# Optimization experiments

Hardware: AMD Instinct MI355X
Metric: run time of the kernel (lower is better)

Reference implementation:

```python
import jax, jax.numpy as jnp
import numpy as np

HEIGHT = 10
IN_DIM = 256
OUT_DIM = 16
BATCH = 65536


def _and_weight(height):
    # Fixed +/-1 tree-structured routing matrix [leaf_nodes, int_nodes]
    int_nodes = 2 ** height - 1
    leaf = 2 ** height
    w = np.zeros((leaf, int_nodes), dtype=np.float32)
    for i in range(height):
        num = 2 ** i
        start = num - 1
        for j in range(start, start + num):
            rb = leaf // num * (j - start)
            rm = rb + leaf // (2 * num)
            re = rb + leaf // num
            w[rb:rm, j] = 1.0
            w[rm:re, j] = -1.0
    return jnp.asarray(w)


def setup_inputs() -> dict:
    key = jax.random.key(0)
    k0, k1, k2, k3 = jax.random.split(key, 4)
    int_nodes = 2 ** HEIGHT - 1
    leaf = 2 ** HEIGHT
    return {
        "x": jax.random.normal(k0, (BATCH, IN_DIM), jnp.float32),
        "W_pred": jax.random.normal(k1, (int_nodes, IN_DIM), jnp.float32) / np.float32(np.sqrt(IN_DIM)),
        "b_pred": jnp.zeros((int_nodes,), jnp.float32),
        "W_or": jax.random.normal(k2, (OUT_DIM, leaf), jnp.float32) / np.float32(np.sqrt(leaf)),
        "action_stds": jax.random.normal(k3, (OUT_DIM, leaf), jnp.float32),
    }


def reference(x, W_pred, b_pred, W_or, action_stds):
    # predicate linear: [B, int_nodes]
    pred_z = x @ W_pred.T + b_pred
    # ScaleBinarizer1 (STE): scale = mean |z| per sample, binarize to {0, fac}
    fac = jax.lax.stop_gradient(jnp.mean(jnp.abs(pred_z), axis=-1, keepdims=True))
    hard = jnp.where(pred_z >= 0, fac, jnp.zeros_like(fac))
    pred_bin = pred_z + jax.lax.stop_gradient(hard - pred_z)  # straight-through
    pred_a = 2.0 * pred_bin - fac  # +/- fac (sign of pred_z scaled)
    # fixed tree AND layer: [B, leaf]
    W_and = _and_weight(HEIGHT)
    and_z = pred_a @ W_and.T
    and_a = jax.nn.softmax(and_z, axis=-1)
    # Sparser1 (STE): hard one-hot of the argmax leaf
    onehot = jax.nn.one_hot(jnp.argmax(and_a, axis=-1), and_a.shape[-1], dtype=and_a.dtype)
    and_a = and_a + jax.lax.stop_gradient(onehot - and_a)
    # OR layer + softmax over classes
    or_z = and_a @ W_or.T  # [B, out_dim]
    out = jax.nn.softmax(or_z, axis=-1)
    # per-action std: sum over leaves of and_a * action_stds, clamped
    std = jnp.clip(jnp.einsum("bl,ol->bo", and_a, action_stds), -20.0, 2.0)
    return out, std
```

## Files before the change

kernel.cpp:

```cpp
#include <hip/hip_runtime.h>
#include <stdint.h>


#define BATCH   65536
#define IN_DIM  256
#define NLEVEL  10
#define NLEAF   1024
#define OUT_DIM 16
#define EPS_TIE 0.02f
#define WB_U32  (1023 * 128)

#define DPP_QUAD_XOR1   0xB1
#define DPP_QUAD_XOR2   0x4E
#define DPP_HALF_MIRROR 0x141

template <int CTRL>
__device__ __forceinline__ float dpp_xfer(float v) {
    return __int_as_float(__builtin_amdgcn_update_dpp(
        0, __float_as_int(v), CTRL, 0xf, 0xf, true));
}
__device__ __forceinline__ float group8_sum(float v) {
    v += dpp_xfer<DPP_QUAD_XOR1>(v);
    v += dpp_xfer<DPP_QUAD_XOR2>(v);
    v += dpp_xfer<DPP_HALF_MIRROR>(v);
    return v;
}
__device__ __forceinline__ float group8_max(float v) {
    v = fmaxf(v, dpp_xfer<DPP_QUAD_XOR1>(v));
    v = fmaxf(v, dpp_xfer<DPP_QUAD_XOR2>(v));
    v = fmaxf(v, dpp_xfer<DPP_HALF_MIRROR>(v));
    return v;
}

__device__ __forceinline__ float blo(uint32_t u) { return __uint_as_float(u << 16); }
__device__ __forceinline__ float bhi(uint32_t u) { return __uint_as_float(u & 0xffff0000u); }

__device__ __forceinline__ uint32_t pkbf(float a, float b) {
    uint32_t ua = __float_as_uint(a), ub = __float_as_uint(b);
    uint32_t ra = (ua + 0x7fffu + ((ua >> 16) & 1u)) >> 16;
    uint32_t rb = (ub + 0x7fffu + ((ub >> 16) & 1u)) >> 16;
    return ra | (rb << 16);
}

__global__ __launch_bounds__(256) void dgt_prep(
    const float* __restrict__ W, uint32_t* __restrict__ Wb)
{
    int i = blockIdx.x * 256 + threadIdx.x;
    if (i < WB_U32) Wb[i] = pkbf(W[2 * i], W[2 * i + 1]);
}

__device__ __forceinline__ int tree_sign_f64(
    const float* __restrict__ xrow, const float* __restrict__ wrow,
    float bias, int l)
{
    double A0 = 0.0, A1 = 0.0, A2 = 0.0, A3 = 0.0;
    #pragma unroll
    for (int k = 0; k < 4; ++k) {
        float4 xa = *reinterpret_cast<const float4*>(xrow + k * 64 + l * 8);
        float4 xb = *reinterpret_cast<const float4*>(xrow + k * 64 + l * 8 + 4);
        float4 wa = *reinterpret_cast<const float4*>(wrow + k * 64 + l * 8);
        float4 wb = *reinterpret_cast<const float4*>(wrow + k * 64 + l * 8 + 4);
        A0 += (double)xa.x * (double)wa.x; A1 += (double)xa.y * (double)wa.y;
        A2 += (double)xa.z * (double)wa.z; A3 += (double)xa.w * (double)wa.w;
        A0 += (double)xb.x * (double)wb.x; A1 += (double)xb.y * (double)wb.y;
        A2 += (double)xb.z * (double)wb.z; A3 += (double)xb.w * (double)wb.w;
    }
    double Z = (A0 + A1) + (A2 + A3);
    #pragma unroll
    for (int off = 4; off > 0; off >>= 1)
        Z += __shfl_xor(Z, off, 64);
    Z += (double)bias;
    return (Z < 0.0) ? 1 : 0;
}

__global__ __launch_bounds__(256, 3) void dgt_b16(
    const float* __restrict__ x,
    const uint32_t* __restrict__ Wb,
    const float* __restrict__ W_pred,
    const float* __restrict__ b_pred,
    const float* __restrict__ W_or,
    const float* __restrict__ a_std,
    float* __restrict__ out)
{
    const int lane = threadIdx.x & 63;
    const int wid  = threadIdx.x >> 6;
    const int l    = lane & 7;
    const int g    = lane >> 3;
    const int sample = blockIdx.x * 32 + wid * 8 + g;

    const float* xrow = x + (size_t)sample * IN_DIM;
    uint32_t p0, p1, p2, p3, p4, p5, p6, p7, p8, p9, p10, p11, p12, p13, p14, p15;
    {
        float4 a0 = *reinterpret_cast<const float4*>(xrow +   0 + l * 8);
        float4 b0 = *reinterpret_cast<const float4*>(xrow +   4 + l * 8);
        float4 a1 = *reinterpret_cast<const float4*>(xrow +  64 + l * 8);
        float4 b1 = *reinterpret_cast<const float4*>(xrow +  68 + l * 8);
        p0 = pkbf(a0.x, a0.y); p1 = pkbf(a0.z, a0.w);
        p2 = pkbf(b0.x, b0.y); p3 = pkbf(b0.z, b0.w);
        p4 = pkbf(a1.x, a1.y); p5 = pkbf(a1.z, a1.w);
        p6 = pkbf(b1.x, b1.y); p7 = pkbf(b1.z, b1.w);
        float4 a2 = *reinterpret_cast<const float4*>(xrow + 128 + l * 8);
        float4 b2 = *reinterpret_cast<const float4*>(xrow + 132 + l * 8);
        float4 a3 = *reinterpret_cast<const float4*>(xrow + 192 + l * 8);
        float4 b3 = *reinterpret_cast<const float4*>(xrow + 196 + l * 8);
        p8  = pkbf(a2.x, a2.y); p9  = pkbf(a2.z, a2.w);
        p10 = pkbf(b2.x, b2.y); p11 = pkbf(b2.z, b2.w);
        p12 = pkbf(a3.x, a3.y); p13 = pkbf(a3.z, a3.w);
        p14 = pkbf(b3.x, b3.y); p15 = pkbf(b3.z, b3.w);
    }

    int node = 0, pos = 0;

    #pragma unroll
    for (int lvl = 0; lvl < NLEVEL; ++lvl) {
        const uint32_t* wb = Wb + (size_t)node * 128;
        float bcur = b_pred[node];

        uint4 A0 = *reinterpret_cast<const uint4*>(wb +  0 + l * 4);
        uint4 A1 = *reinterpret_cast<const uint4*>(wb + 32 + l * 4);
        uint4 B0 = *reinterpret_cast<const uint4*>(wb + 64 + l * 4);
        uint4 B1 = *reinterpret_cast<const uint4*>(wb + 96 + l * 4);

        float a0 = 0.f, a1 = 0.f, a2 = 0.f, a3 = 0.f;
#define FMAU(U, P)                                          \
        a0 += blo(U) * blo(P); a1 += bhi(U) * bhi(P);
#define FMA4(UQ, Pa, Pb, Pc, Pd)                            \
        FMAU(UQ.x, Pa) FMAU(UQ.y, Pb) FMAU(UQ.z, Pc) FMAU(UQ.w, Pd)
        FMA4(A0, p0,  p1,  p2,  p3)
        FMA4(A1, p4,  p5,  p6,  p7)
        FMA4(B0, p8,  p9,  p10, p11)
        FMA4(B1, p12, p13, p14, p15)
#undef FMA4
#undef FMAU

        float z = group8_sum((a0 + a1) + (a2 + a3)) + bcur;

        int right;
        if (__builtin_expect(fabsf(z) >= EPS_TIE, 1))
            right = (z < 0.f) ? 1 : 0;
        else
            right = tree_sign_f64(xrow, W_pred + (size_t)node * IN_DIM,
                                  bcur, l);

        pos  = 2 * pos + right;
        node = 2 * node + 1 + right;
    }
    const int leaf = pos;

    float zx = W_or[(size_t)(2 * l)     * NLEAF + leaf];
    float zy = W_or[(size_t)(2 * l + 1) * NLEAF + leaf];
    float m  = group8_max(fmaxf(zx, zy));
    float ex = __expf(zx - m), ey = __expf(zy - m);
    float s  = group8_sum(ex + ey);
    *reinterpret_cast<float2*>(out + (size_t)sample * OUT_DIM + 2 * l) =
        make_float2(ex / s, ey / s);

    float dx = a_std[(size_t)(2 * l)     * NLEAF + leaf];
    float dy = a_std[(size_t)(2 * l + 1) * NLEAF + leaf];
    *reinterpret_cast<float2*>(out + (size_t)BATCH * OUT_DIM
                               + (size_t)sample * OUT_DIM + 2 * l) =
        make_float2(fminf(fmaxf(dx, -20.f), 2.f),
                    fminf(fmaxf(dy, -20.f), 2.f));
}

__device__ __forceinline__ int tree_sign_f64_r8(
    float4 x0, float4 x1, float4 x2, float4 x3,
    float4 x4, float4 x5, float4 x6, float4 x7,
    const float* wrow, float bias, int l)
{
    double A0 = 0.0, A1 = 0.0, A2 = 0.0, A3 = 0.0;
#define ACC64(K, XV)                                                        \
    {                                                                       \
        float4 w = *reinterpret_cast<const float4*>(wrow + (K)*32 + l * 4); \
        A0 += (double)XV.x * (double)w.x; A1 += (double)XV.y * (double)w.y; \
        A2 += (double)XV.z * (double)w.z; A3 += (double)XV.w * (double)w.w; \
    }
    ACC64(0, x0) ACC64(1, x1) ACC64(2, x2) ACC64(3, x3)
    ACC64(4, x4) ACC64(5, x5) ACC64(6, x6) ACC64(7, x7)
#undef ACC64
    double Z = (A0 + A1) + (A2 + A3);
    #pragma unroll
    for (int off = 4; off > 0; off >>= 1)
        Z += __shfl_xor(Z, off, 64);
    Z += (double)bias;
    return (Z < 0.0) ? 1 : 0;
}

__global__ __launch_bounds__(256, 2) void dgt_f32(
    const float* __restrict__ x,
    const float* __restrict__ W_pred,
    const float* __restrict__ b_pred,
    const float* __restrict__ W_or,
    const float* __restrict__ a_std,
    float* __restrict__ out)
{
    const int lane = threadIdx.x & 63;
    const int wid  = threadIdx.x >> 6;
    const int l    = lane & 7;
    const int g    = lane >> 3;
    const int sample = blockIdx.x * 32 + wid * 8 + g;

    const float* xrow = x + (size_t)sample * IN_DIM;
    float4 x0 = *reinterpret_cast<const float4*>(xrow +   0 + l * 4);
    float4 x1 = *reinterpret_cast<const float4*>(xrow +  32 + l * 4);
    float4 x2 = *reinterpret_cast<const float4*>(xrow +  64 + l * 4);
    float4 x3 = *reinterpret_cast<const float4*>(xrow +  96 + l * 4);
    float4 x4 = *reinterpret_cast<const float4*>(xrow + 128 + l * 4);
    float4 x5 = *reinterpret_cast<const float4*>(xrow + 160 + l * 4);
    float4 x6 = *reinterpret_cast<const float4*>(xrow + 192 + l * 4);
    float4 x7 = *reinterpret_cast<const float4*>(xrow + 224 + l * 4);

    int node = 0, pos = 0;
    float bcur = b_pred[0];
    const float* wrow = W_pred;

    #pragma unroll
    for (int lvl = 0; lvl < NLEVEL; ++lvl) {
        float4 w0 = *reinterpret_cast<const float4*>(wrow +   0 + l * 4);
        float4 w1 = *reinterpret_cast<const float4*>(wrow +  32 + l * 4);
        float4 w2 = *reinterpret_cast<const float4*>(wrow +  64 + l * 4);
        float4 w3 = *reinterpret_cast<const float4*>(wrow +  96 + l * 4);
        float4 w4 = *reinterpret_cast<const float4*>(wrow + 128 + l * 4);
        float4 w5 = *reinterpret_cast<const float4*>(wrow + 160 + l * 4);
        float4 w6 = *reinterpret_cast<const float4*>(wrow + 192 + l * 4);
        float4 w7 = *reinterpret_cast<const float4*>(wrow + 224 + l * 4);

        float bL = 0.f, bR = 0.f;
        if (lvl < NLEVEL - 1) {
            bL = b_pred[2 * node + 1];
            bR = b_pred[2 * node + 2];
        }

        float a0, a1, a2, a3;
        a0  = x0.x * w0.x; a1  = x0.y * w0.y; a2  = x0.z * w0.z; a3  = x0.w * w0.w;
        a0 += x1.x * w1.x; a1 += x1.y * w1.y; a2 += x1.z * w1.z; a3 += x1.w * w1.w;
        a0 += x2.x * w2.x; a1 += x2.y * w2.y; a2 += x2.z * w2.z; a3 += x2.w * w2.w;
        a0 += x3.x * w3.x; a1 += x3.y * w3.y; a2 += x3.z * w3.z; a3 += x3.w * w3.w;
        a0 += x4.x * w4.x; a1 += x4.y * w4.y; a2 += x4.z * w4.z; a3 += x4.w * w4.w;
        a0 += x5.x * w5.x; a1 += x5.y * w5.y; a2 += x5.z * w5.z; a3 += x5.w * w5.w;
        a0 += x6.x * w6.x; a1 += x6.y * w6.y; a2 += x6.z * w6.z; a3 += x6.w * w6.w;
        a0 += x7.x * w7.x; a1 += x7.y * w7.y; a2 += x7.z * w7.z; a3 += x7.w * w7.w;
        float z = group8_sum((a0 + a1) + (a2 + a3)) + bcur;

        int right;
        if (__builtin_expect(fabsf(z) >= 1e-3f, 1))
            right = (z < 0.f) ? 1 : 0;
        else
            right = tree_sign_f64_r8(x0, x1, x2, x3, x4, x5, x6, x7,
                                     wrow, bcur, l);

        pos  = 2 * pos + right;
        node = 2 * node + 1 + right;
        if (lvl < NLEVEL - 1) {
            bcur = right ? bR : bL;
            wrow = W_pred + (size_t)node * IN_DIM;
        }
    }
    const int leaf = pos;

    float zx = W_or[(size_t)(2 * l)     * NLEAF + leaf];
    float zy = W_or[(size_t)(2 * l + 1) * NLEAF + leaf];
    float m  = group8_max(fmaxf(zx, zy));
    float ex = __expf(zx - m), ey = __expf(zy - m);
    float s  = group8_sum(ex + ey);
    *reinterpret_cast<float2*>(out + (size_t)sample * OUT_DIM + 2 * l) =
        make_float2(ex / s, ey / s);

    float dx = a_std[(size_t)(2 * l)     * NLEAF + leaf];
    float dy = a_std[(size_t)(2 * l + 1) * NLEAF + leaf];
    *reinterpret_cast<float2*>(out + (size_t)BATCH * OUT_DIM
                               + (size_t)sample * OUT_DIM + 2 * l) =
        make_float2(fminf(fmaxf(dx, -20.f), 2.f),
                    fminf(fmaxf(dy, -20.f), 2.f));
}

extern "C" void kernel_launch(void* const* d_in, const int* in_sizes, int n_in,
                              void* d_out, int out_size, void* d_ws, size_t ws_size,
                              hipStream_t stream) {
    const float* x      = (const float*)d_in[0];
    const float* W_pred = (const float*)d_in[1];
    const float* b_pred = (const float*)d_in[2];
    const float* W_or   = (const float*)d_in[3];
    const float* a_std  = (const float*)d_in[4];
    float* out = (float*)d_out;

    if (ws_size >= (size_t)WB_U32 * 4) {
        uint32_t* Wb = (uint32_t*)d_ws;
        hipLaunchKernelGGL(dgt_prep, dim3((WB_U32 + 255) / 256), dim3(256),
                           0, stream, W_pred, Wb);
        hipLaunchKernelGGL(dgt_b16, dim3(BATCH / 32), dim3(256), 0, stream,
                           x, Wb, W_pred, b_pred, W_or, a_std, out);
    } else {
        hipLaunchKernelGGL(dgt_f32, dim3(BATCH / 32), dim3(256), 0, stream,
                           x, W_pred, b_pred, W_or, a_std, out);
    }
}
```

Before: 42.34 us.

## Speculatively evaluate both child nodes to traverse two tree levels per hop

The tree descent now handles two levels per iteration. Each hop loads the parent and both child weight rows at once, computes all three dot products, then picks the child result from the parent's sign. This shortens the serial chain of dependent loads from 10 to 5, at the cost of 50% more FMA work and weight traffic, plus more registers (launch bounds lowered from 3 to 2 blocks per CU). The fp64 tie fallback is kept for both the parent and the chosen child.

```diff
diff --git a/kernel.cpp b/kernel.cpp
--- a/kernel.cpp
+++ b/kernel.cpp
@@ -4,7 +4,6 @@
 
 #define BATCH   65536
 #define IN_DIM  256
-#define NLEVEL  10
 #define NLEAF   1024
 #define OUT_DIM 16
 #define EPS_TIE 0.02f
@@ -73,7 +72,15 @@
     return (Z < 0.0) ? 1 : 0;
 }
 
-__global__ __launch_bounds__(256, 3) void dgt_b16(
+__device__ __forceinline__ int guarded_sign(
+    float z, int nd, const float* __restrict__ xrow,
+    const float* __restrict__ W_pred, const float* __restrict__ b_pred, int l)
+{
+    if (__builtin_expect(fabsf(z) >= EPS_TIE, 1)) return (z < 0.f) ? 1 : 0;
+    return tree_sign_f64(xrow, W_pred + (size_t)nd * IN_DIM, b_pred[nd], l);
+}
+
+__global__ __launch_bounds__(256, 2) void dgt_jump(
     const float* __restrict__ x,
     const uint32_t* __restrict__ Wb,
     const float* __restrict__ W_pred,
@@ -112,38 +119,64 @@
     int node = 0, pos = 0;
 
     #pragma unroll
-    for (int lvl = 0; lvl < NLEVEL; ++lvl) {
-        const uint32_t* wb = Wb + (size_t)node * 128;
-        float bcur = b_pred[node];
-
-        uint4 A0 = *reinterpret_cast<const uint4*>(wb +  0 + l * 4);
-        uint4 A1 = *reinterpret_cast<const uint4*>(wb + 32 + l * 4);
-        uint4 B0 = *reinterpret_cast<const uint4*>(wb + 64 + l * 4);
-        uint4 B1 = *reinterpret_cast<const uint4*>(wb + 96 + l * 4);
-
-        float a0 = 0.f, a1 = 0.f, a2 = 0.f, a3 = 0.f;
-#define FMAU(U, P)                                          \
-        a0 += blo(U) * blo(P); a1 += bhi(U) * bhi(P);
-#define FMA4(UQ, Pa, Pb, Pc, Pd)                            \
-        FMAU(UQ.x, Pa) FMAU(UQ.y, Pb) FMAU(UQ.z, Pc) FMAU(UQ.w, Pd)
-        FMA4(A0, p0,  p1,  p2,  p3)
-        FMA4(A1, p4,  p5,  p6,  p7)
-        FMA4(B0, p8,  p9,  p10, p11)
-        FMA4(B1, p12, p13, p14, p15)
+    for (int hop = 0; hop < 5; ++hop) {
+        const int nL = 2 * node + 1, nR = 2 * node + 2;
+        const uint32_t* wP = Wb + (size_t)node * 128;
+        const uint32_t* wL = Wb + (size_t)nL   * 128;
+        const uint32_t* wR = Wb + (size_t)nR   * 128;
+
+        uint4 P0 = *reinterpret_cast<const uint4*>(wP +  0 + l * 4);
+        uint4 P1 = *reinterpret_cast<const uint4*>(wP + 32 + l * 4);
+        uint4 P2 = *reinterpret_cast<const uint4*>(wP + 64 + l * 4);
+        uint4 P3 = *reinterpret_cast<const uint4*>(wP + 96 + l * 4);
+        uint4 L0 = *reinterpret_cast<const uint4*>(wL +  0 + l * 4);
+        uint4 L1 = *reinterpret_cast<const uint4*>(wL + 32 + l * 4);
+        uint4 L2 = *reinterpret_cast<const uint4*>(wL + 64 + l * 4);
+        uint4 L3 = *reinterpret_cast<const uint4*>(wL + 96 + l * 4);
+        uint4 R0 = *reinterpret_cast<const uint4*>(wR +  0 + l * 4);
+        uint4 R1 = *reinterpret_cast<const uint4*>(wR + 32 + l * 4);
+        uint4 R2 = *reinterpret_cast<const uint4*>(wR + 64 + l * 4);
+        uint4 R3 = *reinterpret_cast<const uint4*>(wR + 96 + l * 4);
+
+        float bP = b_pred[node], bL = b_pred[nL], bR = b_pred[nR];
+
+#define FMAU(ACC0, ACC1, U, P)                                   \
+        ACC0 += blo(U) * blo(P); ACC1 += bhi(U) * bhi(P);
+#define FMA4(ACC0, ACC1, ACC2, ACC3, UQ, Pa, Pb, Pc, Pd)         \
+        FMAU(ACC0, ACC1, UQ.x, Pa) FMAU(ACC2, ACC3, UQ.y, Pb)    \
+        FMAU(ACC0, ACC1, UQ.z, Pc) FMAU(ACC2, ACC3, UQ.w, Pd)
+
+        float pa0 = 0.f, pa1 = 0.f, pa2 = 0.f, pa3 = 0.f;
+        FMA4(pa0, pa1, pa2, pa3, P0, p0,  p1,  p2,  p3)
+        FMA4(pa0, pa1, pa2, pa3, P1, p4,  p5,  p6,  p7)
+        FMA4(pa0, pa1, pa2, pa3, P2, p8,  p9,  p10, p11)
+        FMA4(pa0, pa1, pa2, pa3, P3, p12, p13, p14, p15)
+
+        float la0 = 0.f, la1 = 0.f, la2 = 0.f, la3 = 0.f;
+        FMA4(la0, la1, la2, la3, L0, p0,  p1,  p2,  p3)
+        FMA4(la0, la1, la2, la3, L1, p4,  p5,  p6,  p7)
+        FMA4(la0, la1, la2, la3, L2, p8,  p9,  p10, p11)
+        FMA4(la0, la1, la2, la3, L3, p12, p13, p14, p15)
+
+        float ra0 = 0.f, ra1 = 0.f, ra2 = 0.f, ra3 = 0.f;
+        FMA4(ra0, ra1, ra2, ra3, R0, p0,  p1,  p2,  p3)
+        FMA4(ra0, ra1, ra2, ra3, R1, p4,  p5,  p6,  p7)
+        FMA4(ra0, ra1, ra2, ra3, R2, p8,  p9,  p10, p11)
+        FMA4(ra0, ra1, ra2, ra3, R3, p12, p13, p14, p15)
 #undef FMA4
 #undef FMAU
 
-        float z = group8_sum((a0 + a1) + (a2 + a3)) + bcur;
-
-        int right;
-        if (__builtin_expect(fabsf(z) >= EPS_TIE, 1))
-            right = (z < 0.f) ? 1 : 0;
-        else
-            right = tree_sign_f64(xrow, W_pred + (size_t)node * IN_DIM,
-                                  bcur, l);
-
-        pos  = 2 * pos + right;
-        node = 2 * node + 1 + right;
+        float zP = group8_sum((pa0 + pa1) + (pa2 + pa3)) + bP;
+        float zL = group8_sum((la0 + la1) + (la2 + la3)) + bL;
+        float zR = group8_sum((ra0 + ra1) + (ra2 + ra3)) + bR;
+
+        const int rP = guarded_sign(zP, node, xrow, W_pred, b_pred, l);
+        const float zC  = rP ? zR : zL;
+        const int nodeC = 2 * node + 1 + rP;
+        const int rC = guarded_sign(zC, nodeC, xrow, W_pred, b_pred, l);
+
+        pos  = 4 * pos + 2 * rP + rC;
+        node = 2 * nodeC + 1 + rC;
     }
     const int leaf = pos;
 
@@ -215,7 +248,7 @@
     const float* wrow = W_pred;
 
     #pragma unroll
-    for (int lvl = 0; lvl < NLEVEL; ++lvl) {
+    for (int lvl = 0; lvl < 10; ++lvl) {
         float4 w0 = *reinterpret_cast<const float4*>(wrow +   0 + l * 4);
         float4 w1 = *reinterpret_cast<const float4*>(wrow +  32 + l * 4);
         float4 w2 = *reinterpret_cast<const float4*>(wrow +  64 + l * 4);
@@ -226,7 +259,7 @@
         float4 w7 = *reinterpret_cast<const float4*>(wrow + 224 + l * 4);
 
         float bL = 0.f, bR = 0.f;
-        if (lvl < NLEVEL - 1) {
+        if (lvl < 9) {
             bL = b_pred[2 * node + 1];
             bR = b_pred[2 * node + 2];
         }
@@ -251,7 +284,7 @@
 
         pos  = 2 * pos + right;
         node = 2 * node + 1 + right;
-        if (lvl < NLEVEL - 1) {
+        if (lvl < 9) {
             bcur = right ? bR : bL;
             wrow = W_pred + (size_t)node * IN_DIM;
         }
@@ -288,7 +321,7 @@
         uint32_t* Wb = (uint32_t*)d_ws;
         hipLaunchKernelGGL(dgt_prep, dim3((WB_U32 + 255) / 256), dim3(256),
                            0, stream, W_pred, Wb);
-        hipLaunchKernelGGL(dgt_b16, dim3(BATCH / 32), dim3(256), 0, stream,
+        hipLaunchKernelGGL(dgt_jump, dim3(BATCH / 32), dim3(256), 0, stream,
                            x, Wb, W_pred, b_pred, W_or, a_std, out);
     } else {
         hipLaunchKernelGGL(dgt_f32, dim3(BATCH / 32), dim3(256), 0, stream,
```

After: 46.59 us. 10.0% more time.

## Compute top eight tree levels densely with bf16 MFMA into LDS

Applied to the files above, without the earlier changes.

For each block of 64 samples, the predicate values for all 255 nodes of the first eight tree levels are computed with a bf16 16x16x32 MFMA GEMM and staged in shared memory. The per-sample tree walk then reads those levels from LDS and only does the last two levels with gathered dot products. This swaps data-dependent gathered weight rows and per-level DPP reductions for a dense matrix-core GEMM. The cost is far more arithmetic, about 66 KB of LDS per block, and a second read of x.

```diff
diff --git a/kernel.cpp b/kernel.cpp
--- a/kernel.cpp
+++ b/kernel.cpp
@@ -4,11 +4,15 @@
 
 #define BATCH   65536
 #define IN_DIM  256
-#define NLEVEL  10
 #define NLEAF   1024
 #define OUT_DIM 16
 #define EPS_TIE 0.02f
 #define WB_U32  (1023 * 128)
+#define CPAD    260
+
+typedef __attribute__((ext_vector_type(8))) short frag_ab;
+typedef __attribute__((ext_vector_type(4))) float frag_cd;
+union U4F { uint4 u; frag_ab h; };
 
 #define DPP_QUAD_XOR1   0xB1
 #define DPP_QUAD_XOR2   0x4E
@@ -73,7 +77,7 @@
     return (Z < 0.0) ? 1 : 0;
 }
 
-__global__ __launch_bounds__(256, 3) void dgt_b16(
+__global__ __launch_bounds__(512, 2) void dgt_mfma(
     const float* __restrict__ x,
     const uint32_t* __restrict__ Wb,
     const float* __restrict__ W_pred,
@@ -82,14 +86,72 @@
     const float* __restrict__ a_std,
     float* __restrict__ out)
 {
-    const int lane = threadIdx.x & 63;
-    const int wid  = threadIdx.x >> 6;
-    const int l    = lane & 7;
-    const int g    = lane >> 3;
-    const int sample = blockIdx.x * 32 + wid * 8 + g;
-
+    __shared__ float C[64 * CPAD];
+
+    const int tid   = threadIdx.x;
+    const int wave  = tid >> 6;
+    const int lane  = tid & 63;
+    const int mtile = wave & 3;
+    const int nhalf = wave >> 2;
+    const int lr    = lane & 15;
+    const int lk    = lane >> 4;
+
+    frag_cd acc[8];
+    #pragma unroll
+    for (int i = 0; i < 8; ++i) acc[i] = (frag_cd){0.f, 0.f, 0.f, 0.f};
+
+    const float* xa = x + (size_t)(blockIdx.x * 64 + mtile * 16 + lr) * IN_DIM
+                        + lk * 8;
+    #pragma unroll
+    for (int ks = 0; ks < 8; ++ks) {
+        float4 fa = *reinterpret_cast<const float4*>(xa + ks * 32);
+        float4 fb = *reinterpret_cast<const float4*>(xa + ks * 32 + 4);
+        U4F a;
+        a.u.x = pkbf(fa.x, fa.y); a.u.y = pkbf(fa.z, fa.w);
+        a.u.z = pkbf(fb.x, fb.y); a.u.w = pkbf(fb.z, fb.w);
+        #pragma unroll
+        for (int nt = 0; nt < 8; ++nt) {
+            const int node = (nhalf * 8 + nt) * 16 + lr;
+            U4F b;
+            b.u = *reinterpret_cast<const uint4*>(
+                Wb + (size_t)node * 128 + ks * 16 + lk * 4);
+            acc[nt] = __builtin_amdgcn_mfma_f32_16x16x32_bf16(
+                a.h, b.h, acc[nt], 0, 0, 0);
+        }
+    }
+    #pragma unroll
+    for (int nt = 0; nt < 8; ++nt) {
+        const int n  = (nhalf * 8 + nt) * 16 + lr;
+        const float bn = b_pred[n];
+        #pragma unroll
+        for (int r = 0; r < 4; ++r) {
+            const int s = mtile * 16 + lk * 4 + r;
+            C[s * CPAD + n] = acc[nt][r] + bn;
+        }
+    }
+    __syncthreads();
+
+    const int g = tid >> 3;
+    const int l = tid & 7;
+    const int sample = blockIdx.x * 64 + g;
     const float* xrow = x + (size_t)sample * IN_DIM;
-    uint32_t p0, p1, p2, p3, p4, p5, p6, p7, p8, p9, p10, p11, p12, p13, p14, p15;
+
+    int node = 0, pos = 0;
+    #pragma unroll
+    for (int lvl = 0; lvl < 8; ++lvl) {
+        float z = C[g * CPAD + node];
+        int right;
+        if (__builtin_expect(fabsf(z) >= EPS_TIE, 1))
+            right = (z < 0.f) ? 1 : 0;
+        else
+            right = tree_sign_f64(xrow, W_pred + (size_t)node * IN_DIM,
+                                  b_pred[node], l);
+        pos  = 2 * pos + right;
+        node = 2 * node + 1 + right;
+    }
+
+    uint32_t p0, p1, p2, p3, p4, p5, p6, p7,
+             p8, p9, p10, p11, p12, p13, p14, p15;
     {
         float4 a0 = *reinterpret_cast<const float4*>(xrow +   0 + l * 8);
         float4 b0 = *reinterpret_cast<const float4*>(xrow +   4 + l * 8);
@@ -109,13 +171,10 @@
         p14 = pkbf(b3.x, b3.y); p15 = pkbf(b3.z, b3.w);
     }
 
-    int node = 0, pos = 0;
-
-    #pragma unroll
-    for (int lvl = 0; lvl < NLEVEL; ++lvl) {
+    #pragma unroll
+    for (int lvl = 8; lvl < 10; ++lvl) {
         const uint32_t* wb = Wb + (size_t)node * 128;
         float bcur = b_pred[node];
-
         uint4 A0 = *reinterpret_cast<const uint4*>(wb +  0 + l * 4);
         uint4 A1 = *reinterpret_cast<const uint4*>(wb + 32 + l * 4);
         uint4 B0 = *reinterpret_cast<const uint4*>(wb + 64 + l * 4);
@@ -132,7 +191,6 @@
         FMA4(B1, p12, p13, p14, p15)
 #undef FMA4
 #undef FMAU
-
         float z = group8_sum((a0 + a1) + (a2 + a3)) + bcur;
 
         int right;
@@ -141,7 +199,6 @@
         else
             right = tree_sign_f64(xrow, W_pred + (size_t)node * IN_DIM,
                                   bcur, l);
-
         pos  = 2 * pos + right;
         node = 2 * node + 1 + right;
     }
@@ -215,7 +272,7 @@
     const float* wrow = W_pred;
 
     #pragma unroll
-    for (int lvl = 0; lvl < NLEVEL; ++lvl) {
+    for (int lvl = 0; lvl < 10; ++lvl) {
         float4 w0 = *reinterpret_cast<const float4*>(wrow +   0 + l * 4);
         float4 w1 = *reinterpret_cast<const float4*>(wrow +  32 + l * 4);
         float4 w2 = *reinterpret_cast<const float4*>(wrow +  64 + l * 4);
@@ -226,7 +283,7 @@
         float4 w7 = *reinterpret_cast<const float4*>(wrow + 224 + l * 4);
 
         float bL = 0.f, bR = 0.f;
-        if (lvl < NLEVEL - 1) {
+        if (lvl < 9) {
             bL = b_pred[2 * node + 1];
             bR = b_pred[2 * node + 2];
         }
@@ -251,7 +308,7 @@
 
         pos  = 2 * pos + right;
         node = 2 * node + 1 + right;
-        if (lvl < NLEVEL - 1) {
+        if (lvl < 9) {
             bcur = right ? bR : bL;
             wrow = W_pred + (size_t)node * IN_DIM;
         }
@@ -288,7 +345,7 @@
         uint32_t* Wb = (uint32_t*)d_ws;
         hipLaunchKernelGGL(dgt_prep, dim3((WB_U32 + 255) / 256), dim3(256),
                            0, stream, W_pred, Wb);
-        hipLaunchKernelGGL(dgt_b16, dim3(BATCH / 32), dim3(256), 0, stream,
+        hipLaunchKernelGGL(dgt_mfma, dim3(BATCH / 64), dim3(512), 0, stream,
                            x, Wb, W_pred, b_pred, W_or, a_std, out);
     } else {
         hipLaunchKernelGGL(dgt_f32, dim3(BATCH / 32), dim3(256), 0, stream,
```

New measurement: 97.37 us. 130% more time.
